# Optimization experiments

Measured on AMD Instinct MI355X. Metric: run time of the kernel, lower is better.

Reference implementation:

```python
import jax, jax.numpy as jnp
import numpy as np

SPARSE_SHAPE = (41, 1600, 1408)  # (D, H, W), batch_size = 1
N_VOXELS = 200000
BN_EPS = 1e-3


def _kernel_offsets():
    # 27 offsets of a 3x3x3 kernel, padding=1 -> offsets in {-1,0,1}^3
    g = np.stack(np.meshgrid(*([np.arange(-1, 2)] * 3), indexing='ij'), axis=-1)
    return jnp.asarray(g.reshape(-1, 3), dtype=jnp.int32)  # (27, 3)


def _neighbor_map(coords):
    """Submanifold rulebook: for each active voxel and each of 27 offsets,
    index of the active neighbor voxel, or N (sentinel) if inactive/out-of-bounds."""
    D, H, W = SPARSE_SHAPE
    N = coords.shape[0]
    b, z, y, x = coords[:, 0], coords[:, 1], coords[:, 2], coords[:, 3]
    flat = ((b * D + z) * H + y) * W + x  # batch_size=1
    grid = jnp.full((D * H * W,), N, dtype=jnp.int32).at[flat].set(
        jnp.arange(N, dtype=jnp.int32))
    offs = _kernel_offsets()                      # (27, 3)
    nc = coords[:, None, 1:4] + offs[None]        # (N, 27, 3)
    lim = jnp.asarray([D, H, W], dtype=jnp.int32)
    valid = jnp.all((nc >= 0) & (nc < lim), axis=-1)  # (N, 27)
    nflat = ((b[:, None] * D + nc[..., 0]) * H + nc[..., 1]) * W + nc[..., 2]
    nbr = jnp.where(valid, grid[jnp.where(valid, nflat, 0)], N)
    return nbr  # (N, 27) int32, sentinel = N


def _subm_conv(features, nbr, w):
    # gather -> batched small GEMM -> (implicit) scatter back to same voxels
    pad = jnp.concatenate(
        [features, jnp.zeros((1, features.shape[1]), features.dtype)], axis=0)
    gathered = pad[nbr]                           # (N, 27, Cin)
    return jnp.einsum('nkc,kcd->nd', gathered, w)  # (N, Cout)


def _bn_relu(x, gamma, beta):
    # BatchNorm1d in train mode over the voxel (batch) dim, eps=1e-3
    mean = x.mean(axis=0)
    var = x.var(axis=0)
    return jax.nn.relu((x - mean) * jax.lax.rsqrt(var + BN_EPS) * gamma + beta)


def setup_inputs() -> dict:
    D, H, W = SPARSE_SHAPE
    total = D * H * W
    rng = np.random.default_rng(0)
    # unique active voxel locations
    flat = np.unique(rng.integers(0, total, size=N_VOXELS + 20000))
    rng.shuffle(flat)
    flat = flat[:N_VOXELS]
    assert flat.shape[0] == N_VOXELS
    z = flat // (H * W)
    y = (flat // W) % H
    x = flat % W
    b = np.zeros_like(z)
    coords = jnp.asarray(np.stack([b, z, y, x], axis=1), dtype=jnp.int32)

    key = jax.random.key(0)
    k0, k1, k2 = jax.random.split(key, 3)
    features = jax.random.uniform(k0, (N_VOXELS, 3), dtype=jnp.float32)
    w1 = jax.random.normal(k1, (27, 3, 16), dtype=jnp.float32) * 0.1
    w2 = jax.random.normal(k2, (27, 16, 16), dtype=jnp.float32) * 0.05
    return {
        'features': features, 'coords': coords,
        'w1': w1, 'gamma1': jnp.ones(16, jnp.float32), 'beta1': jnp.zeros(16, jnp.float32),
        'w2': w2, 'gamma2': jnp.ones(16, jnp.float32), 'beta2': jnp.zeros(16, jnp.float32),
    }


def reference(features, coords, w1, gamma1, beta1, w2, gamma2, beta2):
    nbr = _neighbor_map(coords)   # shared indice_key='subm1' -> reused by both convs
    h = _bn_relu(_subm_conv(features, nbr, w1), gamma1, beta1)
    h = _bn_relu(_subm_conv(h, nbr, w2), gamma2, beta2)
    return h
```

## Files before the change

kernel.cpp:

```cpp
#include <hip/hip_runtime.h>
#include <stdint.h>

#define SPARSE_D 41
#define SPARSE_H 1600
#define SPARSE_W 1408
#define BN_EPS 0.001f

static constexpr int NYB = SPARSE_H / 2;
static constexpr int NBUCKET = SPARSE_D * NYB;
static constexpr int PCAP = 12;


__global__ void k_insert(const int* __restrict__ coords, const float* __restrict__ feat,
                         uint32_t* __restrict__ bent, float* __restrict__ featp, int N) {
    int n = blockIdx.x * blockDim.x + threadIdx.x;
    if (n >= N) return;
    int4 c4 = ((const int4*)coords)[n];
    int z = c4.y, y = c4.z, x = c4.w;
    int b = z * NYB + (y >> 1);
    uint32_t e = ((uint32_t)(y & 1) << 29) | ((uint32_t)x << 18) | (uint32_t)n;
    int slot = atomicAdd((int*)&bent[(size_t)b * 32], 1) + 1;
    if (slot <= 31) bent[(size_t)b * 32 + slot] = e;
    float f0 = feat[n * 3 + 0], f1 = feat[n * 3 + 1], f2 = feat[n * 3 + 2];
    ((float4*)featp)[n] = make_float4(f0, f1, f2, 0.f);
}

__device__ __forceinline__ void stats_epilogue(const float acc[16],
                                               float* __restrict__ partials,
                                               float (*sred)[32]) {
    int lid = threadIdx.x & 63;
    int wid = threadIdx.x >> 6;
    #pragma unroll
    for (int d = 0; d < 16; ++d) {
        float v = acc[d];
        float v2 = v * v;
        #pragma unroll
        for (int off = 32; off; off >>= 1) {
            v += __shfl_xor(v, off);
            v2 += __shfl_xor(v2, off);
        }
        if (lid == 0) { sred[wid][d] = v; sred[wid][16 + d] = v2; }
    }
    __syncthreads();
    if (threadIdx.x < 32)
        partials[(size_t)blockIdx.x * 32 + threadIdx.x] =
            sred[0][threadIdx.x] + sred[1][threadIdx.x] +
            sred[2][threadIdx.x] + sred[3][threadIdx.x];
}

__global__ void k_build_conv1(const int* __restrict__ coords, const uint32_t* __restrict__ bent,
                              const float* __restrict__ featp, const float* __restrict__ w1,
                              int* __restrict__ pcnt, uint32_t* __restrict__ pairs,
                              float* __restrict__ h1, float* __restrict__ partials, int N) {
    __shared__ float sred[4][32];
    __shared__ float sw1[27 * 52];
    for (int i = threadIdx.x; i < 27 * 48; i += 256)
        sw1[(i / 48) * 52 + (i % 48)] = w1[i];
    __syncthreads();

    int n = blockIdx.x * blockDim.x + threadIdx.x;
    float acc[16];
    #pragma unroll
    for (int d = 0; d < 16; ++d) acc[d] = 0.f;
    if (n < N) {
        int4 c4 = ((const int4*)coords)[n];
        int z = c4.y, y = c4.z, x = c4.w;

        float4 f = ((const float4*)featp)[n];
        const float* wd = w1 + 13 * 48;
        #pragma unroll
        for (int d = 0; d < 16; ++d)
            acc[d] = fmaf(f.x, wd[d], fmaf(f.y, wd[16 + d], f.z * wd[32 + d]));

        int yb0 = (y - 1) >> 1;
        uint4 q0[6];
        int bix[6], mm[6];
        #pragma unroll
        for (int p = 0; p < 6; ++p) {
            int zz = z + p / 2 - 1;
            int yb = yb0 + (p & 1);
            bool v = ((unsigned)zz < SPARSE_D) & ((unsigned)yb < NYB);
            int b = v ? (zz * NYB + yb) : 0;
            bix[p] = b;
            q0[p] = *(const uint4*)&bent[(size_t)b * 32];
            mm[p] = v ? 1 : 0;
        }

        uint32_t lpairs[PCAP];
        int cnt = 0;
        #pragma unroll
        for (int p = 0; p < 6; ++p) {
            int m = mm[p] ? min((int)q0[p].x, 31) : 0;
            int yb = yb0 + (p & 1);
            int dzk = (p / 2) * 9;
            auto scan_entry = [&](uint32_t e, int slot) {
                if (slot > m) return;
                int ey = (yb << 1) + (int)(e >> 29);
                int ex = (int)((e >> 18) & 0x7FFu);
                int dy = ey - y, dx = ex - x;
                if ((unsigned)(dy + 1) > 2u || (unsigned)(dx + 1) > 2u) return;
                uint32_t idx = e & 0x3FFFFu;
                if (idx == (uint32_t)n) return;
                int k = dzk + (dy + 1) * 3 + (dx + 1);
                if (cnt < PCAP) lpairs[cnt] = ((uint32_t)k << 18) | idx;
                ++cnt;
            };
            scan_entry(q0[p].y, 1);
            scan_entry(q0[p].z, 2);
            scan_entry(q0[p].w, 3);
            for (int w = 4; w <= m; w += 4) {
                uint4 q = *(const uint4*)&bent[(size_t)bix[p] * 32 + w];
                scan_entry(q.x, w);
                scan_entry(q.y, w + 1);
                scan_entry(q.z, w + 2);
                scan_entry(q.w, w + 3);
            }
        }
        cnt = min(cnt, PCAP);
        pcnt[n] = cnt;
        for (int c = 0; c < cnt; ++c) {
            uint32_t pr = lpairs[c];
            pairs[(size_t)c * N + n] = pr;
            int k = (int)(pr >> 18), idx = (int)(pr & 0x3FFFFu);
            float4 g = ((const float4*)featp)[idx];
            const float* wk = &sw1[k * 52];
            #pragma unroll
            for (int d = 0; d < 16; ++d)
                acc[d] = fmaf(g.x, wk[d], fmaf(g.y, wk[16 + d], fmaf(g.z, wk[32 + d], acc[d])));
        }
        float4* o = (float4*)&h1[(size_t)n * 16];
        o[0] = make_float4(acc[0], acc[1], acc[2], acc[3]);
        o[1] = make_float4(acc[4], acc[5], acc[6], acc[7]);
        o[2] = make_float4(acc[8], acc[9], acc[10], acc[11]);
        o[3] = make_float4(acc[12], acc[13], acc[14], acc[15]);
    }
    stats_epilogue(acc, partials, sred);
}

__global__ void k_conv2(const float* __restrict__ h1, const int* __restrict__ pcnt,
                        const uint32_t* __restrict__ pairs, const float* __restrict__ w2,
                        const float* __restrict__ scsh1, float* __restrict__ out,
                        float* __restrict__ partials, int N) {
    __shared__ float sred[4][32];
    __shared__ float sc[16], sh[16];
    __shared__ float sw2[27 * 260];
    if (threadIdx.x < 16) { sc[threadIdx.x] = scsh1[threadIdx.x]; sh[threadIdx.x] = scsh1[16 + threadIdx.x]; }
    for (int i = threadIdx.x; i < 27 * 256; i += 256)
        sw2[(i >> 8) * 260 + (i & 255)] = w2[i];
    __syncthreads();

    int n = blockIdx.x * blockDim.x + threadIdx.x;
    float acc[16];
    #pragma unroll
    for (int d = 0; d < 16; ++d) acc[d] = 0.f;
    if (n < N) {
        float g[16];
        #pragma unroll
        for (int c = 0; c < 16; c += 4) {
            float4 t = *(const float4*)&h1[(size_t)n * 16 + c];
            g[c]     = fmaxf(fmaf(t.x, sc[c],     sh[c]),     0.f);
            g[c + 1] = fmaxf(fmaf(t.y, sc[c + 1], sh[c + 1]), 0.f);
            g[c + 2] = fmaxf(fmaf(t.z, sc[c + 2], sh[c + 2]), 0.f);
            g[c + 3] = fmaxf(fmaf(t.w, sc[c + 3], sh[c + 3]), 0.f);
        }
        {
            const float* w = w2 + 13 * 256;
            #pragma unroll
            for (int c = 0; c < 16; ++c)
                #pragma unroll
                for (int d = 0; d < 16; ++d)
                    acc[d] = fmaf(g[c], w[c * 16 + d], acc[d]);
        }
        int m = min(pcnt[n], PCAP);
        for (int cc = 0; cc < m; ++cc) {
            uint32_t pr = pairs[(size_t)cc * N + n];
            int k = (int)(pr >> 18), idx = (int)(pr & 0x3FFFFu);
            #pragma unroll
            for (int c = 0; c < 16; c += 4) {
                float4 t = *(const float4*)&h1[(size_t)idx * 16 + c];
                g[c]     = fmaxf(fmaf(t.x, sc[c],     sh[c]),     0.f);
                g[c + 1] = fmaxf(fmaf(t.y, sc[c + 1], sh[c + 1]), 0.f);
                g[c + 2] = fmaxf(fmaf(t.z, sc[c + 2], sh[c + 2]), 0.f);
                g[c + 3] = fmaxf(fmaf(t.w, sc[c + 3], sh[c + 3]), 0.f);
            }
            const float* wk = &sw2[k * 260];
            #pragma unroll
            for (int c = 0; c < 16; ++c)
                #pragma unroll
                for (int d = 0; d < 16; ++d)
                    acc[d] = fmaf(g[c], wk[c * 16 + d], acc[d]);
        }
        float4* o = (float4*)&out[(size_t)n * 16];
        o[0] = make_float4(acc[0], acc[1], acc[2], acc[3]);
        o[1] = make_float4(acc[4], acc[5], acc[6], acc[7]);
        o[2] = make_float4(acc[8], acc[9], acc[10], acc[11]);
        o[3] = make_float4(acc[12], acc[13], acc[14], acc[15]);
    }
    stats_epilogue(acc, partials, sred);
}

__global__ void k_finalize(const float* __restrict__ partials, int nb,
                           const float* __restrict__ gamma, const float* __restrict__ beta,
                           float* __restrict__ scsh, float invN) {
    __shared__ float red[32][33];
    int ch = threadIdx.x & 31;
    int rg = threadIdx.x >> 5;
    float s0 = 0.f, s1 = 0.f, s2 = 0.f, s3 = 0.f;
    int j = rg;
    for (; j + 96 < nb; j += 128) {
        s0 += partials[(size_t)(j      ) * 32 + ch];
        s1 += partials[(size_t)(j + 32 ) * 32 + ch];
        s2 += partials[(size_t)(j + 64 ) * 32 + ch];
        s3 += partials[(size_t)(j + 96 ) * 32 + ch];
    }
    for (; j < nb; j += 32) s0 += partials[(size_t)j * 32 + ch];
    red[rg][ch] = (s0 + s1) + (s2 + s3);
    __syncthreads();
    if (threadIdx.x < 32) {
        float t = 0.f;
        #pragma unroll
        for (int r = 0; r < 32; ++r) t += red[r][threadIdx.x];
        red[0][threadIdx.x] = t;
    }
    __syncthreads();
    if (threadIdx.x < 16) {
        int d = threadIdx.x;
        float mean = red[0][d] * invN;
        float var = red[0][16 + d] * invN - mean * mean;
        float s2c = gamma[d] * rsqrtf(var + BN_EPS);
        scsh[d] = s2c;
        scsh[16 + d] = beta[d] - mean * s2c;
    }
}

__global__ void k_bnrelu4(float* __restrict__ x, const float* __restrict__ scsh, int nvec) {
    __shared__ float sc[16], sh[16];
    if (threadIdx.x < 16) { sc[threadIdx.x] = scsh[threadIdx.x]; sh[threadIdx.x] = scsh[16 + threadIdx.x]; }
    __syncthreads();
    int i = blockIdx.x * blockDim.x + threadIdx.x;
    if (i < nvec) {
        float4 v = ((float4*)x)[i];
        int c0 = (i & 3) * 4;
        v.x = fmaxf(fmaf(v.x, sc[c0 + 0], sh[c0 + 0]), 0.f);
        v.y = fmaxf(fmaf(v.y, sc[c0 + 1], sh[c0 + 1]), 0.f);
        v.z = fmaxf(fmaf(v.z, sc[c0 + 2], sh[c0 + 2]), 0.f);
        v.w = fmaxf(fmaf(v.w, sc[c0 + 3], sh[c0 + 3]), 0.f);
        ((float4*)x)[i] = v;
    }
}

extern "C" void kernel_launch(void* const* d_in, const int* in_sizes, int n_in,
                              void* d_out, int out_size, void* d_ws, size_t ws_size,
                              hipStream_t stream) {
    const float* feat   = (const float*)d_in[0];
    const int*   coords = (const int*)d_in[1];
    const float* w1     = (const float*)d_in[2];
    const float* gamma1 = (const float*)d_in[3];
    const float* beta1  = (const float*)d_in[4];
    const float* w2     = (const float*)d_in[5];
    const float* gamma2 = (const float*)d_in[6];
    const float* beta2  = (const float*)d_in[7];
    float* out = (float*)d_out;
    const int N = in_sizes[0] / 3;

    const int T = 256;
    const int nb = (N + T - 1) / T;
    const int nvec = N * 16 / 4;
    const int nbv = (nvec + T - 1) / T;

    char* ws = (char*)d_ws;
    size_t off = 0;
    uint32_t* bent = (uint32_t*)(ws + off);  off += (size_t)NBUCKET * 32 * 4;
    int* pcnt = (int*)(ws + off);            off += ((size_t)N * 4 + 63) & ~(size_t)63;
    uint32_t* pairs = (uint32_t*)(ws + off); off += (size_t)PCAP * N * 4;
    float* h1 = (float*)(ws + off);          off += (size_t)N * 16 * 4;
    float* featp = (float*)(ws + off);       off += (size_t)N * 4 * 4;
    float* partials = (float*)(ws + off);    off += ((size_t)nb * 32 * 4 + 63) & ~(size_t)63;
    float* stats = (float*)(ws + off);

    hipMemsetAsync(bent, 0, (size_t)NBUCKET * 32 * 4, stream);
    k_insert<<<nb, T, 0, stream>>>(coords, feat, bent, featp, N);
    k_build_conv1<<<nb, T, 0, stream>>>(coords, bent, featp, w1, pcnt, pairs, h1, partials, N);
    k_finalize<<<1, 1024, 0, stream>>>(partials, nb, gamma1, beta1, stats, 1.f / (float)N);
    k_conv2<<<nb, T, 0, stream>>>(h1, pcnt, pairs, w2, stats, out, partials, N);
    k_finalize<<<1, 1024, 0, stream>>>(partials, nb, gamma2, beta2, stats + 32, 1.f / (float)N);
    k_bnrelu4<<<nbv, T, 0, stream>>>(out, stats + 32, nvec);
}
```

Measured before the change: 151.8 us.

## Fold BN stat finalize into consumer kernels, removing separate finalize launches

```diff
diff --git a/kernel.cpp b/kernel.cpp
--- a/kernel.cpp
+++ b/kernel.cpp
@@ -46,6 +46,42 @@
         partials[(size_t)blockIdx.x * 32 + threadIdx.x] =
             sred[0][threadIdx.x] + sred[1][threadIdx.x] +
             sred[2][threadIdx.x] + sred[3][threadIdx.x];
+}
+
+__device__ __forceinline__ void reduce_scsh(const float* __restrict__ partials, int nbk,
+                                            const float* __restrict__ gamma,
+                                            const float* __restrict__ beta,
+                                            float invN, float* __restrict__ sc,
+                                            float* __restrict__ sh) {
+    __shared__ float red[8][33];
+    int ch = threadIdx.x & 31, rg = threadIdx.x >> 5;
+    float s0 = 0.f, s1 = 0.f, s2 = 0.f, s3 = 0.f;
+    int j = rg;
+    for (; j + 24 < nbk; j += 32) {
+        s0 += partials[(size_t)(j     ) * 32 + ch];
+        s1 += partials[(size_t)(j +  8) * 32 + ch];
+        s2 += partials[(size_t)(j + 16) * 32 + ch];
+        s3 += partials[(size_t)(j + 24) * 32 + ch];
+    }
+    for (; j < nbk; j += 8) s0 += partials[(size_t)j * 32 + ch];
+    red[rg][ch] = (s0 + s1) + (s2 + s3);
+    __syncthreads();
+    if (threadIdx.x < 32) {
+        float t = 0.f;
+        #pragma unroll
+        for (int r = 0; r < 8; ++r) t += red[r][threadIdx.x];
+        red[0][threadIdx.x] = t;
+    }
+    __syncthreads();
+    if (threadIdx.x < 16) {
+        int d = threadIdx.x;
+        float mean = red[0][d] * invN;
+        float var  = red[0][16 + d] * invN - mean * mean;
+        float s2c  = gamma[d] * rsqrtf(var + BN_EPS);
+        sc[d] = s2c;
+        sh[d] = beta[d] - mean * s2c;
+    }
+    __syncthreads();
 }
 
 __global__ void k_build_conv1(const int* __restrict__ coords, const uint32_t* __restrict__ bent,
@@ -139,15 +175,16 @@
 
 __global__ void k_conv2(const float* __restrict__ h1, const int* __restrict__ pcnt,
                         const uint32_t* __restrict__ pairs, const float* __restrict__ w2,
-                        const float* __restrict__ scsh1, float* __restrict__ out,
+                        const float* __restrict__ p1, int nbk,
+                        const float* __restrict__ gamma1, const float* __restrict__ beta1,
+                        float invN, float* __restrict__ out,
                         float* __restrict__ partials, int N) {
     __shared__ float sred[4][32];
     __shared__ float sc[16], sh[16];
     __shared__ float sw2[27 * 260];
-    if (threadIdx.x < 16) { sc[threadIdx.x] = scsh1[threadIdx.x]; sh[threadIdx.x] = scsh1[16 + threadIdx.x]; }
     for (int i = threadIdx.x; i < 27 * 256; i += 256)
         sw2[(i >> 8) * 260 + (i & 255)] = w2[i];
-    __syncthreads();
+    reduce_scsh(p1, nbk, gamma1, beta1, invN, sc, sh);
 
     int n = blockIdx.x * blockDim.x + threadIdx.x;
     float acc[16];
@@ -199,46 +236,13 @@
     stats_epilogue(acc, partials, sred);
 }
 
-__global__ void k_finalize(const float* __restrict__ partials, int nb,
-                           const float* __restrict__ gamma, const float* __restrict__ beta,
-                           float* __restrict__ scsh, float invN) {
-    __shared__ float red[32][33];
-    int ch = threadIdx.x & 31;
-    int rg = threadIdx.x >> 5;
-    float s0 = 0.f, s1 = 0.f, s2 = 0.f, s3 = 0.f;
-    int j = rg;
-    for (; j + 96 < nb; j += 128) {
-        s0 += partials[(size_t)(j      ) * 32 + ch];
-        s1 += partials[(size_t)(j + 32 ) * 32 + ch];
-        s2 += partials[(size_t)(j + 64 ) * 32 + ch];
-        s3 += partials[(size_t)(j + 96 ) * 32 + ch];
-    }
-    for (; j < nb; j += 32) s0 += partials[(size_t)j * 32 + ch];
-    red[rg][ch] = (s0 + s1) + (s2 + s3);
-    __syncthreads();
-    if (threadIdx.x < 32) {
-        float t = 0.f;
-        #pragma unroll
-        for (int r = 0; r < 32; ++r) t += red[r][threadIdx.x];
-        red[0][threadIdx.x] = t;
-    }
-    __syncthreads();
-    if (threadIdx.x < 16) {
-        int d = threadIdx.x;
-        float mean = red[0][d] * invN;
-        float var = red[0][16 + d] * invN - mean * mean;
-        float s2c = gamma[d] * rsqrtf(var + BN_EPS);
-        scsh[d] = s2c;
-        scsh[16 + d] = beta[d] - mean * s2c;
-    }
-}
-
-__global__ void k_bnrelu4(float* __restrict__ x, const float* __restrict__ scsh, int nvec) {
+__global__ void k_bnrelu_fin(float* __restrict__ x, const float* __restrict__ p2, int nbk,
+                             const float* __restrict__ gamma2, const float* __restrict__ beta2,
+                             float invN, int nvec) {
     __shared__ float sc[16], sh[16];
-    if (threadIdx.x < 16) { sc[threadIdx.x] = scsh[threadIdx.x]; sh[threadIdx.x] = scsh[16 + threadIdx.x]; }
-    __syncthreads();
-    int i = blockIdx.x * blockDim.x + threadIdx.x;
-    if (i < nvec) {
+    reduce_scsh(p2, nbk, gamma2, beta2, invN, sc, sh);
+    int G = (int)gridDim.x * (int)blockDim.x;
+    for (int i = blockIdx.x * blockDim.x + threadIdx.x; i < nvec; i += G) {
         float4 v = ((float4*)x)[i];
         int c0 = (i & 3) * 4;
         v.x = fmaxf(fmaf(v.x, sc[c0 + 0], sh[c0 + 0]), 0.f);
@@ -266,7 +270,7 @@
     const int T = 256;
     const int nb = (N + T - 1) / T;
     const int nvec = N * 16 / 4;
-    const int nbv = (nvec + T - 1) / T;
+    const float invN = 1.f / (float)N;
 
     char* ws = (char*)d_ws;
     size_t off = 0;
@@ -275,14 +279,13 @@
     uint32_t* pairs = (uint32_t*)(ws + off); off += (size_t)PCAP * N * 4;
     float* h1 = (float*)(ws + off);          off += (size_t)N * 16 * 4;
     float* featp = (float*)(ws + off);       off += (size_t)N * 4 * 4;
-    float* partials = (float*)(ws + off);    off += ((size_t)nb * 32 * 4 + 63) & ~(size_t)63;
-    float* stats = (float*)(ws + off);
+    float* p1 = (float*)(ws + off);          off += ((size_t)nb * 32 * 4 + 63) & ~(size_t)63;
+    float* p2 = (float*)(ws + off);          off += ((size_t)nb * 32 * 4 + 63) & ~(size_t)63;
 
     hipMemsetAsync(bent, 0, (size_t)NBUCKET * 32 * 4, stream);
     k_insert<<<nb, T, 0, stream>>>(coords, feat, bent, featp, N);
-    k_build_conv1<<<nb, T, 0, stream>>>(coords, bent, featp, w1, pcnt, pairs, h1, partials, N);
-    k_finalize<<<1, 1024, 0, stream>>>(partials, nb, gamma1, beta1, stats, 1.f / (float)N);
-    k_conv2<<<nb, T, 0, stream>>>(h1, pcnt, pairs, w2, stats, out, partials, N);
-    k_finalize<<<1, 1024, 0, stream>>>(partials, nb, gamma2, beta2, stats + 32, 1.f / (float)N);
-    k_bnrelu4<<<nbv, T, 0, stream>>>(out, stats + 32, nvec);
-}
+    k_build_conv1<<<nb, T, 0, stream>>>(coords, bent, featp, w1, pcnt, pairs, h1, p1, N);
+    k_conv2<<<nb, T, 0, stream>>>(h1, pcnt, pairs, w2, p1, nb, gamma1, beta1, invN,
+                                  out, p2, N);
+    k_bnrelu_fin<<<nb, T, 0, stream>>>(out, p2, nb, gamma2, beta2, invN, nvec);
+}
```

Result: slower. 162.0 us (+6.7%).

## Split output channels across two threads per voxel in both conv kernels

Applied to the files above, without the earlier changes.

```diff
diff --git a/kernel.cpp b/kernel.cpp
--- a/kernel.cpp
+++ b/kernel.cpp
@@ -25,21 +25,21 @@
     ((float4*)featp)[n] = make_float4(f0, f1, f2, 0.f);
 }
 
-__device__ __forceinline__ void stats_epilogue(const float acc[16],
-                                               float* __restrict__ partials,
-                                               float (*sred)[32]) {
+__device__ __forceinline__ void stats_epilogue8(const float acc[8],
+                                                float* __restrict__ partials,
+                                                float (*sred)[32]) {
     int lid = threadIdx.x & 63;
     int wid = threadIdx.x >> 6;
     #pragma unroll
-    for (int d = 0; d < 16; ++d) {
+    for (int d = 0; d < 8; ++d) {
         float v = acc[d];
         float v2 = v * v;
         #pragma unroll
-        for (int off = 32; off; off >>= 1) {
+        for (int off = 32; off >= 2; off >>= 1) {
             v += __shfl_xor(v, off);
             v2 += __shfl_xor(v2, off);
         }
-        if (lid == 0) { sred[wid][d] = v; sred[wid][16 + d] = v2; }
+        if (lid < 2) { sred[wid][lid * 8 + d] = v; sred[wid][16 + lid * 8 + d] = v2; }
     }
     __syncthreads();
     if (threadIdx.x < 32)
@@ -58,18 +58,20 @@
         sw1[(i / 48) * 52 + (i % 48)] = w1[i];
     __syncthreads();
 
-    int n = blockIdx.x * blockDim.x + threadIdx.x;
-    float acc[16];
+    int t = blockIdx.x * blockDim.x + threadIdx.x;
+    int n = t >> 1;
+    int d0 = (t & 1) * 8;
+    float acc[8];
     #pragma unroll
-    for (int d = 0; d < 16; ++d) acc[d] = 0.f;
+    for (int d = 0; d < 8; ++d) acc[d] = 0.f;
     if (n < N) {
         int4 c4 = ((const int4*)coords)[n];
         int z = c4.y, y = c4.z, x = c4.w;
 
         float4 f = ((const float4*)featp)[n];
-        const float* wd = w1 + 13 * 48;
-        #pragma unroll
-        for (int d = 0; d < 16; ++d)
+        const float* wd = &sw1[13 * 52 + d0];
+        #pragma unroll
+        for (int d = 0; d < 8; ++d)
             acc[d] = fmaf(f.x, wd[d], fmaf(f.y, wd[16 + d], f.z * wd[32 + d]));
 
         int yb0 = (y - 1) >> 1;
@@ -117,24 +119,22 @@
             }
         }
         cnt = min(cnt, PCAP);
-        pcnt[n] = cnt;
+        if (!d0) pcnt[n] = cnt;
         for (int c = 0; c < cnt; ++c) {
             uint32_t pr = lpairs[c];
-            pairs[(size_t)c * N + n] = pr;
+            if (!d0) pairs[(size_t)c * N + n] = pr;
             int k = (int)(pr >> 18), idx = (int)(pr & 0x3FFFFu);
             float4 g = ((const float4*)featp)[idx];
-            const float* wk = &sw1[k * 52];
-            #pragma unroll
-            for (int d = 0; d < 16; ++d)
+            const float* wk = &sw1[k * 52 + d0];
+            #pragma unroll
+            for (int d = 0; d < 8; ++d)
                 acc[d] = fmaf(g.x, wk[d], fmaf(g.y, wk[16 + d], fmaf(g.z, wk[32 + d], acc[d])));
         }
-        float4* o = (float4*)&h1[(size_t)n * 16];
+        float4* o = (float4*)&h1[(size_t)n * 16 + d0];
         o[0] = make_float4(acc[0], acc[1], acc[2], acc[3]);
         o[1] = make_float4(acc[4], acc[5], acc[6], acc[7]);
-        o[2] = make_float4(acc[8], acc[9], acc[10], acc[11]);
-        o[3] = make_float4(acc[12], acc[13], acc[14], acc[15]);
-    }
-    stats_epilogue(acc, partials, sred);
+    }
+    stats_epilogue8(acc, partials, sred);
 }
 
 __global__ void k_conv2(const float* __restrict__ h1, const int* __restrict__ pcnt,
@@ -149,27 +149,29 @@
         sw2[(i >> 8) * 260 + (i & 255)] = w2[i];
     __syncthreads();
 
-    int n = blockIdx.x * blockDim.x + threadIdx.x;
-    float acc[16];
+    int t = blockIdx.x * blockDim.x + threadIdx.x;
+    int n = t >> 1;
+    int d0 = (t & 1) * 8;
+    float acc[8];
     #pragma unroll
-    for (int d = 0; d < 16; ++d) acc[d] = 0.f;
+    for (int d = 0; d < 8; ++d) acc[d] = 0.f;
     if (n < N) {
         float g[16];
         #pragma unroll
         for (int c = 0; c < 16; c += 4) {
-            float4 t = *(const float4*)&h1[(size_t)n * 16 + c];
-            g[c]     = fmaxf(fmaf(t.x, sc[c],     sh[c]),     0.f);
-            g[c + 1] = fmaxf(fmaf(t.y, sc[c + 1], sh[c + 1]), 0.f);
-            g[c + 2] = fmaxf(fmaf(t.z, sc[c + 2], sh[c + 2]), 0.f);
-            g[c + 3] = fmaxf(fmaf(t.w, sc[c + 3], sh[c + 3]), 0.f);
+            float4 tv = *(const float4*)&h1[(size_t)n * 16 + c];
+            g[c]     = fmaxf(fmaf(tv.x, sc[c],     sh[c]),     0.f);
+            g[c + 1] = fmaxf(fmaf(tv.y, sc[c + 1], sh[c + 1]), 0.f);
+            g[c + 2] = fmaxf(fmaf(tv.z, sc[c + 2], sh[c + 2]), 0.f);
+            g[c + 3] = fmaxf(fmaf(tv.w, sc[c + 3], sh[c + 3]), 0.f);
         }
         {
-            const float* w = w2 + 13 * 256;
+            const float* wk = &sw2[13 * 260 + d0];
             #pragma unroll
             for (int c = 0; c < 16; ++c)
                 #pragma unroll
-                for (int d = 0; d < 16; ++d)
-                    acc[d] = fmaf(g[c], w[c * 16 + d], acc[d]);
+                for (int d = 0; d < 8; ++d)
+                    acc[d] = fmaf(g[c], wk[c * 16 + d], acc[d]);
         }
         int m = min(pcnt[n], PCAP);
         for (int cc = 0; cc < m; ++cc) {
@@ -177,26 +179,24 @@
             int k = (int)(pr >> 18), idx = (int)(pr & 0x3FFFFu);
             #pragma unroll
             for (int c = 0; c < 16; c += 4) {
-                float4 t = *(const float4*)&h1[(size_t)idx * 16 + c];
-                g[c]     = fmaxf(fmaf(t.x, sc[c],     sh[c]),     0.f);
-                g[c + 1] = fmaxf(fmaf(t.y, sc[c + 1], sh[c + 1]), 0.f);
-                g[c + 2] = fmaxf(fmaf(t.z, sc[c + 2], sh[c + 2]), 0.f);
-                g[c + 3] = fmaxf(fmaf(t.w, sc[c + 3], sh[c + 3]), 0.f);
+                float4 tv = *(const float4*)&h1[(size_t)idx * 16 + c];
+                g[c]     = fmaxf(fmaf(tv.x, sc[c],     sh[c]),     0.f);
+                g[c + 1] = fmaxf(fmaf(tv.y, sc[c + 1], sh[c + 1]), 0.f);
+                g[c + 2] = fmaxf(fmaf(tv.z, sc[c + 2], sh[c + 2]), 0.f);
+                g[c + 3] = fmaxf(fmaf(tv.w, sc[c + 3], sh[c + 3]), 0.f);
             }
-            const float* wk = &sw2[k * 260];
+            const float* wk = &sw2[k * 260 + d0];
             #pragma unroll
             for (int c = 0; c < 16; ++c)
                 #pragma unroll
-                for (int d = 0; d < 16; ++d)
+                for (int d = 0; d < 8; ++d)
                     acc[d] = fmaf(g[c], wk[c * 16 + d], acc[d]);
         }
-        float4* o = (float4*)&out[(size_t)n * 16];
+        float4* o = (float4*)&out[(size_t)n * 16 + d0];
         o[0] = make_float4(acc[0], acc[1], acc[2], acc[3]);
         o[1] = make_float4(acc[4], acc[5], acc[6], acc[7]);
-        o[2] = make_float4(acc[8], acc[9], acc[10], acc[11]);
-        o[3] = make_float4(acc[12], acc[13], acc[14], acc[15]);
-    }
-    stats_epilogue(acc, partials, sred);
+    }
+    stats_epilogue8(acc, partials, sred);
 }
 
 __global__ void k_finalize(const float* __restrict__ partials, int nb,
@@ -264,7 +264,8 @@
     const int N = in_sizes[0] / 3;
 
     const int T = 256;
-    const int nb = (N + T - 1) / T;
+    const int nb  = (N + T - 1) / T;
+    const int nb2 = (2 * N + T - 1) / T;
     const int nvec = N * 16 / 4;
     const int nbv = (nvec + T - 1) / T;
 
@@ -275,14 +276,14 @@
     uint32_t* pairs = (uint32_t*)(ws + off); off += (size_t)PCAP * N * 4;
     float* h1 = (float*)(ws + off);          off += (size_t)N * 16 * 4;
     float* featp = (float*)(ws + off);       off += (size_t)N * 4 * 4;
-    float* partials = (float*)(ws + off);    off += ((size_t)nb * 32 * 4 + 63) & ~(size_t)63;
+    float* partials = (float*)(ws + off);    off += ((size_t)nb2 * 32 * 4 + 63) & ~(size_t)63;
     float* stats = (float*)(ws + off);
 
     hipMemsetAsync(bent, 0, (size_t)NBUCKET * 32 * 4, stream);
     k_insert<<<nb, T, 0, stream>>>(coords, feat, bent, featp, N);
-    k_build_conv1<<<nb, T, 0, stream>>>(coords, bent, featp, w1, pcnt, pairs, h1, partials, N);
-    k_finalize<<<1, 1024, 0, stream>>>(partials, nb, gamma1, beta1, stats, 1.f / (float)N);
-    k_conv2<<<nb, T, 0, stream>>>(h1, pcnt, pairs, w2, stats, out, partials, N);
-    k_finalize<<<1, 1024, 0, stream>>>(partials, nb, gamma2, beta2, stats + 32, 1.f / (float)N);
+    k_build_conv1<<<nb2, T, 0, stream>>>(coords, bent, featp, w1, pcnt, pairs, h1, partials, N);
+    k_finalize<<<1, 1024, 0, stream>>>(partials, nb2, gamma1, beta1, stats, 1.f / (float)N);
+    k_conv2<<<nb2, T, 0, stream>>>(h1, pcnt, pairs, w2, stats, out, partials, N);
+    k_finalize<<<1, 1024, 0, stream>>>(partials, nb2, gamma2, beta2, stats + 32, 1.f / (float)N);
     k_bnrelu4<<<nbv, T, 0, stream>>>(out, stats + 32, nvec);
 }
```

After: 156.7 us. 3.2% more time.

## Reorder voxels spatially via counting sort and swizzle blocks across XCDs

Applied to the files above, without the earlier changes.

```diff
diff --git a/kernel.cpp b/kernel.cpp
--- a/kernel.cpp
+++ b/kernel.cpp
@@ -11,22 +11,79 @@
 static constexpr int PCAP = 12;
 
 
-__global__ void k_insert(const int* __restrict__ coords, const float* __restrict__ feat,
-                         uint32_t* __restrict__ bent, float* __restrict__ featp, int N) {
+__global__ void k_insert(const int* __restrict__ coords, uint32_t* __restrict__ cnts,
+                         uint32_t* __restrict__ slotarr, int N) {
     int n = blockIdx.x * blockDim.x + threadIdx.x;
     if (n >= N) return;
     int4 c4 = ((const int4*)coords)[n];
+    int z = c4.y, y = c4.z;
+    int b = z * NYB + (y >> 1);
+    int slot = (int)atomicAdd(&cnts[b], 1u) + 1;
+    slotarr[n] = ((uint32_t)b << 6) | (uint32_t)min(slot, 32);
+}
+
+__global__ void k_scan(const uint32_t* __restrict__ cnts, uint32_t* __restrict__ bent2,
+                       int* __restrict__ base, int NB) {
+    __shared__ int ps[1024];
+    int tid = threadIdx.x;
+    const int CH = (NB + 1023) / 1024;
+    int b0 = tid * CH;
+    int sum = 0;
+    for (int j = 0; j < CH; ++j) {
+        int b = b0 + j;
+        if (b < NB) {
+            int c = (int)cnts[b];
+            bent2[(size_t)b * 32] = (uint32_t)c;
+            sum += min(c, 31);
+        }
+    }
+    ps[tid] = sum;
+    __syncthreads();
+    for (int off = 1; off < 1024; off <<= 1) {
+        int v = (tid >= off) ? ps[tid - off] : 0;
+        __syncthreads();
+        ps[tid] += v;
+        __syncthreads();
+    }
+    int run = ps[tid] - sum;
+    for (int j = 0; j < CH; ++j) {
+        int b = b0 + j;
+        if (b < NB) { base[b] = run; run += min((int)cnts[b], 31); }
+    }
+    if (tid == 1023) { base[NB] = ps[1023]; base[NB + 1] = 0; }
+}
+
+__global__ void k_permute(const int* __restrict__ coords, const float* __restrict__ feat,
+                          const uint32_t* __restrict__ slotarr, int* __restrict__ base,
+                          uint32_t* __restrict__ bent2, uint32_t* __restrict__ czarr,
+                          int* __restrict__ orig, float* __restrict__ featp, int NB, int N) {
+    int n = blockIdx.x * blockDim.x + threadIdx.x;
+    if (n >= N) return;
+    uint32_t sv = slotarr[n];
+    int b = (int)(sv >> 6), s = (int)(sv & 63u);
+    int4 c4 = ((const int4*)coords)[n];
     int z = c4.y, y = c4.z, x = c4.w;
-    int b = z * NYB + (y >> 1);
-    uint32_t e = ((uint32_t)(y & 1) << 29) | ((uint32_t)x << 18) | (uint32_t)n;
-    int slot = atomicAdd((int*)&bent[(size_t)b * 32], 1) + 1;
-    if (slot <= 31) bent[(size_t)b * 32 + slot] = e;
+    int v;
+    if (s <= 31) {
+        v = base[b] + s - 1;
+        bent2[(size_t)b * 32 + s] = ((uint32_t)(y & 1) << 29) | ((uint32_t)x << 18) | (uint32_t)v;
+    } else {
+        v = base[NB] + atomicAdd((uint32_t*)&base[NB + 1], 1u);
+    }
+    czarr[v] = ((uint32_t)z << 22) | ((uint32_t)y << 11) | (uint32_t)x;
+    orig[v] = n;
     float f0 = feat[n * 3 + 0], f1 = feat[n * 3 + 1], f2 = feat[n * 3 + 2];
-    ((float4*)featp)[n] = make_float4(f0, f1, f2, 0.f);
+    ((float4*)featp)[v] = make_float4(f0, f1, f2, 0.f);
+}
+
+__device__ __forceinline__ int xcd_swz(int o, int nwg) {
+    int q = nwg >> 3, r = nwg & 7;
+    int x = o & 7, i = o >> 3;
+    return (x < r ? x * (q + 1) : r * (q + 1) + (x - r) * q) + i;
 }
 
 __device__ __forceinline__ void stats_epilogue(const float acc[16],
-                                               float* __restrict__ partials,
+                                               float* __restrict__ partials, int blk,
                                                float (*sred)[32]) {
     int lid = threadIdx.x & 63;
     int wid = threadIdx.x >> 6;
@@ -43,12 +100,12 @@
     }
     __syncthreads();
     if (threadIdx.x < 32)
-        partials[(size_t)blockIdx.x * 32 + threadIdx.x] =
+        partials[(size_t)blk * 32 + threadIdx.x] =
             sred[0][threadIdx.x] + sred[1][threadIdx.x] +
             sred[2][threadIdx.x] + sred[3][threadIdx.x];
 }
 
-__global__ void k_build_conv1(const int* __restrict__ coords, const uint32_t* __restrict__ bent,
+__global__ void k_build_conv1(const uint32_t* __restrict__ czarr, const uint32_t* __restrict__ bent2,
                               const float* __restrict__ featp, const float* __restrict__ w1,
                               int* __restrict__ pcnt, uint32_t* __restrict__ pairs,
                               float* __restrict__ h1, float* __restrict__ partials, int N) {
@@ -58,15 +115,16 @@
         sw1[(i / 48) * 52 + (i % 48)] = w1[i];
     __syncthreads();
 
-    int n = blockIdx.x * blockDim.x + threadIdx.x;
+    int blk = xcd_swz(blockIdx.x, (int)gridDim.x);
+    int v = blk * (int)blockDim.x + (int)threadIdx.x;
     float acc[16];
     #pragma unroll
     for (int d = 0; d < 16; ++d) acc[d] = 0.f;
-    if (n < N) {
-        int4 c4 = ((const int4*)coords)[n];
-        int z = c4.y, y = c4.z, x = c4.w;
-
-        float4 f = ((const float4*)featp)[n];
+    if (v < N) {
+        uint32_t cz = czarr[v];
+        int z = (int)(cz >> 22), y = (int)((cz >> 11) & 0x7FFu), x = (int)(cz & 0x7FFu);
+
+        float4 f = ((const float4*)featp)[v];
         const float* wd = w1 + 13 * 48;
         #pragma unroll
         for (int d = 0; d < 16; ++d)
@@ -79,11 +137,11 @@
         for (int p = 0; p < 6; ++p) {
             int zz = z + p / 2 - 1;
             int yb = yb0 + (p & 1);
-            bool v = ((unsigned)zz < SPARSE_D) & ((unsigned)yb < NYB);
-            int b = v ? (zz * NYB + yb) : 0;
+            bool ok = ((unsigned)zz < SPARSE_D) & ((unsigned)yb < NYB);
+            int b = ok ? (zz * NYB + yb) : 0;
             bix[p] = b;
-            q0[p] = *(const uint4*)&bent[(size_t)b * 32];
-            mm[p] = v ? 1 : 0;
+            q0[p] = *(const uint4*)&bent2[(size_t)b * 32];
+            mm[p] = ok ? 1 : 0;
         }
 
         uint32_t lpairs[PCAP];
@@ -100,7 +158,7 @@
                 int dy = ey - y, dx = ex - x;
                 if ((unsigned)(dy + 1) > 2u || (unsigned)(dx + 1) > 2u) return;
                 uint32_t idx = e & 0x3FFFFu;
-                if (idx == (uint32_t)n) return;
+                if (idx == (uint32_t)v) return;
                 int k = dzk + (dy + 1) * 3 + (dx + 1);
                 if (cnt < PCAP) lpairs[cnt] = ((uint32_t)k << 18) | idx;
                 ++cnt;
@@ -109,7 +167,7 @@
             scan_entry(q0[p].z, 2);
             scan_entry(q0[p].w, 3);
             for (int w = 4; w <= m; w += 4) {
-                uint4 q = *(const uint4*)&bent[(size_t)bix[p] * 32 + w];
+                uint4 q = *(const uint4*)&bent2[(size_t)bix[p] * 32 + w];
                 scan_entry(q.x, w);
                 scan_entry(q.y, w + 1);
                 scan_entry(q.z, w + 2);
@@ -117,10 +175,10 @@
             }
         }
         cnt = min(cnt, PCAP);
-        pcnt[n] = cnt;
+        pcnt[v] = cnt;
         for (int c = 0; c < cnt; ++c) {
             uint32_t pr = lpairs[c];
-            pairs[(size_t)c * N + n] = pr;
+            pairs[(size_t)c * N + v] = pr;
             int k = (int)(pr >> 18), idx = (int)(pr & 0x3FFFFu);
             float4 g = ((const float4*)featp)[idx];
             const float* wk = &sw1[k * 52];
@@ -128,19 +186,19 @@
             for (int d = 0; d < 16; ++d)
                 acc[d] = fmaf(g.x, wk[d], fmaf(g.y, wk[16 + d], fmaf(g.z, wk[32 + d], acc[d])));
         }
-        float4* o = (float4*)&h1[(size_t)n * 16];
+        float4* o = (float4*)&h1[(size_t)v * 16];
         o[0] = make_float4(acc[0], acc[1], acc[2], acc[3]);
         o[1] = make_float4(acc[4], acc[5], acc[6], acc[7]);
         o[2] = make_float4(acc[8], acc[9], acc[10], acc[11]);
         o[3] = make_float4(acc[12], acc[13], acc[14], acc[15]);
     }
-    stats_epilogue(acc, partials, sred);
+    stats_epilogue(acc, partials, blk, sred);
 }
 
 __global__ void k_conv2(const float* __restrict__ h1, const int* __restrict__ pcnt,
                         const uint32_t* __restrict__ pairs, const float* __restrict__ w2,
-                        const float* __restrict__ scsh1, float* __restrict__ out,
-                        float* __restrict__ partials, int N) {
+                        const float* __restrict__ scsh1, const int* __restrict__ orig,
+                        float* __restrict__ out, float* __restrict__ partials, int N) {
     __shared__ float sred[4][32];
     __shared__ float sc[16], sh[16];
     __shared__ float sw2[27 * 260];
@@ -149,15 +207,16 @@
         sw2[(i >> 8) * 260 + (i & 255)] = w2[i];
     __syncthreads();
 
-    int n = blockIdx.x * blockDim.x + threadIdx.x;
+    int blk = xcd_swz(blockIdx.x, (int)gridDim.x);
+    int v = blk * (int)blockDim.x + (int)threadIdx.x;
     float acc[16];
     #pragma unroll
     for (int d = 0; d < 16; ++d) acc[d] = 0.f;
-    if (n < N) {
+    if (v < N) {
         float g[16];
         #pragma unroll
         for (int c = 0; c < 16; c += 4) {
-            float4 t = *(const float4*)&h1[(size_t)n * 16 + c];
+            float4 t = *(const float4*)&h1[(size_t)v * 16 + c];
             g[c]     = fmaxf(fmaf(t.x, sc[c],     sh[c]),     0.f);
             g[c + 1] = fmaxf(fmaf(t.y, sc[c + 1], sh[c + 1]), 0.f);
             g[c + 2] = fmaxf(fmaf(t.z, sc[c + 2], sh[c + 2]), 0.f);
@@ -171,9 +230,9 @@
                 for (int d = 0; d < 16; ++d)
                     acc[d] = fmaf(g[c], w[c * 16 + d], acc[d]);
         }
-        int m = min(pcnt[n], PCAP);
+        int m = min(pcnt[v], PCAP);
         for (int cc = 0; cc < m; ++cc) {
-            uint32_t pr = pairs[(size_t)cc * N + n];
+            uint32_t pr = pairs[(size_t)cc * N + v];
             int k = (int)(pr >> 18), idx = (int)(pr & 0x3FFFFu);
             #pragma unroll
             for (int c = 0; c < 16; c += 4) {
@@ -190,13 +249,13 @@
                 for (int d = 0; d < 16; ++d)
                     acc[d] = fmaf(g[c], wk[c * 16 + d], acc[d]);
         }
-        float4* o = (float4*)&out[(size_t)n * 16];
+        float4* o = (float4*)&out[(size_t)orig[v] * 16];
         o[0] = make_float4(acc[0], acc[1], acc[2], acc[3]);
         o[1] = make_float4(acc[4], acc[5], acc[6], acc[7]);
         o[2] = make_float4(acc[8], acc[9], acc[10], acc[11]);
         o[3] = make_float4(acc[12], acc[13], acc[14], acc[15]);
     }
-    stats_epilogue(acc, partials, sred);
+    stats_epilogue(acc, partials, blk, sred);
 }
 
 __global__ void k_finalize(const float* __restrict__ partials, int nb,
@@ -267,22 +326,31 @@
     const int nb = (N + T - 1) / T;
     const int nvec = N * 16 / 4;
     const int nbv = (nvec + T - 1) / T;
+    const float invN = 1.f / (float)N;
 
     char* ws = (char*)d_ws;
     size_t off = 0;
-    uint32_t* bent = (uint32_t*)(ws + off);  off += (size_t)NBUCKET * 32 * 4;
-    int* pcnt = (int*)(ws + off);            off += ((size_t)N * 4 + 63) & ~(size_t)63;
+    uint32_t* cnts  = (uint32_t*)(ws + off); off += ((size_t)NBUCKET * 4 + 63) & ~(size_t)63;
+    int* base       = (int*)(ws + off);      off += ((size_t)(NBUCKET + 2) * 4 + 63) & ~(size_t)63;
+    uint32_t* bent2 = (uint32_t*)(ws + off); off += (size_t)NBUCKET * 32 * 4;
+    uint32_t* slotarr = (uint32_t*)(ws + off); off += (size_t)N * 4;
+    uint32_t* czarr = (uint32_t*)(ws + off); off += (size_t)N * 4;
+    int* orig       = (int*)(ws + off);      off += (size_t)N * 4;
+    int* pcnt       = (int*)(ws + off);      off += ((size_t)N * 4 + 63) & ~(size_t)63;
     uint32_t* pairs = (uint32_t*)(ws + off); off += (size_t)PCAP * N * 4;
-    float* h1 = (float*)(ws + off);          off += (size_t)N * 16 * 4;
-    float* featp = (float*)(ws + off);       off += (size_t)N * 4 * 4;
+    float* h1       = (float*)(ws + off);    off += (size_t)N * 16 * 4;
+    float* featp    = (float*)(ws + off);    off += (size_t)N * 4 * 4;
     float* partials = (float*)(ws + off);    off += ((size_t)nb * 32 * 4 + 63) & ~(size_t)63;
-    float* stats = (float*)(ws + off);
-
-    hipMemsetAsync(bent, 0, (size_t)NBUCKET * 32 * 4, stream);
-    k_insert<<<nb, T, 0, stream>>>(coords, feat, bent, featp, N);
-    k_build_conv1<<<nb, T, 0, stream>>>(coords, bent, featp, w1, pcnt, pairs, h1, partials, N);
-    k_finalize<<<1, 1024, 0, stream>>>(partials, nb, gamma1, beta1, stats, 1.f / (float)N);
-    k_conv2<<<nb, T, 0, stream>>>(h1, pcnt, pairs, w2, stats, out, partials, N);
-    k_finalize<<<1, 1024, 0, stream>>>(partials, nb, gamma2, beta2, stats + 32, 1.f / (float)N);
+    float* stats    = (float*)(ws + off);
+
+    hipMemsetAsync(cnts, 0, (size_t)NBUCKET * 4, stream);
+    k_insert<<<nb, T, 0, stream>>>(coords, cnts, slotarr, N);
+    k_scan<<<1, 1024, 0, stream>>>(cnts, bent2, base, NBUCKET);
+    k_permute<<<nb, T, 0, stream>>>(coords, feat, slotarr, base, bent2, czarr, orig, featp,
+                                    NBUCKET, N);
+    k_build_conv1<<<nb, T, 0, stream>>>(czarr, bent2, featp, w1, pcnt, pairs, h1, partials, N);
+    k_finalize<<<1, 1024, 0, stream>>>(partials, nb, gamma1, beta1, stats, invN);
+    k_conv2<<<nb, T, 0, stream>>>(h1, pcnt, pairs, w2, stats, orig, out, partials, N);
+    k_finalize<<<1, 1024, 0, stream>>>(partials, nb, gamma2, beta2, stats + 32, invN);
     k_bnrelu4<<<nbv, T, 0, stream>>>(out, stats + 32, nvec);
 }
```

After: 237.0 us. 1.56x slower.
